# Kernel optimization log

Hardware: AMD Instinct MI355X
Metric: run time of the kernel (lower is better)

## Reference

```python
import jax, jax.numpy as jnp
import numpy as np

EPS = 1e-6

def _layernorm(x):
    mu = jnp.mean(x, axis=-1, keepdims=True)
    var = jnp.mean(jnp.square(x - mu), axis=-1, keepdims=True)
    return (x - mu) / jnp.sqrt(var + EPS)

def setup_inputs() -> dict:
    key = jax.random.key(0)
    ks = jax.random.split(key, 12)
    B, N, C = 4, 1024, 1024
    H = 16
    Dff = 4 * C
    s = 0.02
    x = jax.random.normal(ks[0], (B, N, C), dtype=jnp.float32)
    mask = jax.random.randint(ks[1], (N, N), 0, 2) > 0  # True = attend
    wq = jax.random.normal(ks[2], (C, C), dtype=jnp.float32) * s
    bq = jnp.zeros((C,), dtype=jnp.float32)
    wkv = jax.random.normal(ks[3], (C, 2 * C), dtype=jnp.float32) * s
    bkv = jnp.zeros((2 * C,), dtype=jnp.float32)
    wo = jax.random.normal(ks[4], (C, C), dtype=jnp.float32) * s
    bo = jnp.zeros((C,), dtype=jnp.float32)
    w1 = jax.random.normal(ks[5], (C, Dff), dtype=jnp.float32) * s
    b1 = jnp.zeros((Dff,), dtype=jnp.float32)
    w2 = jax.random.normal(ks[6], (Dff, C), dtype=jnp.float32) * s
    b2 = jnp.zeros((C,), dtype=jnp.float32)
    return {"x": x, "mask": mask, "wq": wq, "bq": bq, "wkv": wkv, "bkv": bkv,
            "wo": wo, "bo": bo, "w1": w1, "b1": b1, "w2": w2, "b2": b2}

def reference(x, mask, wq, bq, wkv, bkv, wo, bo, w1, b1, w2, b2):
    B, N, C = x.shape
    H = 16
    d = C // H
    scale = d ** -0.5
    max_neg = -jnp.finfo(x.dtype).max
    # attn_bias: 0 where mask True, -max where False; broadcast [1,1,N,N]
    attn_bias = jnp.where(mask, jnp.asarray(0.0, x.dtype), jnp.asarray(max_neg, x.dtype))[None, None]

    # --- pre-norm attention ---
    xn = _layernorm(x)
    q = (xn @ wq + bq).reshape(B, N, H, d)
    kv = xn @ wkv + bkv
    k, v = jnp.split(kv, 2, axis=-1)
    k = k.reshape(B, N, H, d)
    v = v.reshape(B, N, H, d)
    sim = jnp.einsum('bihd,bjhd->bhij', q, k) * scale + attn_bias
    attn = jax.nn.softmax(sim, axis=-1)
    o = jnp.einsum('bhij,bjhd->bihd', attn, v).reshape(B, N, C)
    x = x + (o @ wo + bo)

    # --- pre-norm MLP with tanh-approx GELU ---
    xn = _layernorm(x)
    h = jax.nn.gelu(xn @ w1 + b1, approximate=True)
    x = x + (h @ w2 + b2)
    return x
```

## Files before the change

kernel.cpp:

```cpp
#include <hip/hip_runtime.h>
#include <hip/hip_bf16.h>

typedef short bf16x8 __attribute__((ext_vector_type(8)));
typedef float f32x4 __attribute__((ext_vector_type(4)));
typedef unsigned short u16x8 __attribute__((ext_vector_type(8)));

#define MFMA16(a,b,c) __builtin_amdgcn_mfma_f32_16x16x32_bf16((a),(b),(c),0,0,0)

__device__ inline unsigned short f32_to_bf16(float f){
  union { float f; unsigned u; } v; v.f = f;
  unsigned u = v.u;
  u += 0x7FFFu + ((u >> 16) & 1u);
  return (unsigned short)(u >> 16);
}
__device__ inline float bf16_to_f32(unsigned short u){
  union { unsigned u; float f; } v; v.u = ((unsigned)u)<<16; return v.f;
}

__device__ inline float gelu_tanh(float x){
  float x3 = x*x*x;
  float t = tanhf(0.7978845608028654f*(x + 0.044715f*x3));
  return 0.5f*x*(1.0f+t);
}

__device__ inline void gload16(const void* g, void* l){
  __builtin_amdgcn_global_load_lds(
      (const __attribute__((address_space(1))) void*)g,
      (__attribute__((address_space(3))) void*)l, 16, 0, 0);
}

__device__ inline int xcd_swz(int lin, int nwg){
  int cpx = nwg >> 3;
  return (lin & 7)*cpx + (lin >> 3);
}

__global__ void detect_mask_kernel(const unsigned* __restrict__ m, int* __restrict__ flag){
  __shared__ int s;
  if (threadIdx.x == 0) s = 0;
  __syncthreads();
  unsigned w = m[threadIdx.x];
  if (w > 1u) atomicOr(&s, 1);
  __syncthreads();
  if (threadIdx.x == 0) *flag = s;
}

__global__ __launch_bounds__(256) void mask_bias_kernel(
    const void* __restrict__ mask, const int* __restrict__ flag,
    unsigned short* __restrict__ biasr){
  __shared__ float mt[16][64];
  int qg = blockIdx.x, jt = blockIdx.y;
  int t = threadIdx.x;
  int fl = *flag;
  int jc = jt*64 + (t&63);
  #pragma unroll
  for (int k2=0;k2<4;k2++){
    int qr = qg*16 + (t>>6) + k2*4;
    bool a = fl ? (((const unsigned char*)mask)[(size_t)qr*1024 + jc] != 0)
                : (((const int*)mask)[(size_t)qr*1024 + jc] != 0);
    mt[(t>>6)+k2*4][t&63] = a ? -23.083120654223414f : -1e30f;
  }
  __syncthreads();
  ushort4 ob;
  unsigned short tmp[4];
  #pragma unroll
  for (int u=0;u<4;u++){
    int p = t*4+u;
    int e = p&15, lane = p>>4;
    int i = e>>2, jj = e&3;
    int ln2 = lane&15, g2 = lane>>4;
    tmp[u] = f32_to_bf16(mt[g2*4+i][jj*16+ln2]);
  }
  ob.x=tmp[0]; ob.y=tmp[1]; ob.z=tmp[2]; ob.w=tmp[3];
  *(ushort4*)&biasr[((size_t)(qg*16+jt)*64)*16 + t*4] = ob;
}

__global__ __launch_bounds__(256) void transpose_cvt_kernel(
    const float* __restrict__ W, unsigned short* __restrict__ WT, int K, int N){
  __shared__ float tile[32][37];
  int n0 = blockIdx.x*32, k0 = blockIdx.y*32;
  int r = threadIdx.x>>3, c4 = threadIdx.x&7;
  float4 v = *(const float4*)&W[(size_t)(k0+r)*N + n0 + c4*4];
  tile[r][c4*4+0]=v.x; tile[r][c4*4+1]=v.y; tile[r][c4*4+2]=v.z; tile[r][c4*4+3]=v.w;
  __syncthreads();
  ushort4 o;
  o.x = f32_to_bf16(tile[c4*4+0][r]);
  o.y = f32_to_bf16(tile[c4*4+1][r]);
  o.z = f32_to_bf16(tile[c4*4+2][r]);
  o.w = f32_to_bf16(tile[c4*4+3][r]);
  *(ushort4*)&WT[(size_t)(n0+r)*K + k0 + c4*4] = o;
}

__global__ __launch_bounds__(256) void vtrans_kernel(
    const unsigned short* __restrict__ qkv, unsigned short* __restrict__ vt){
  __shared__ unsigned short t[32][33];
  int b = blockIdx.z;
  int n0 = blockIdx.x*32, d0 = blockIdx.y*32;
  int tx = threadIdx.x & 31, ty = threadIdx.x >> 5;
  #pragma unroll
  for (int r=0;r<4;r++)
    t[ty+8*r][tx] = qkv[(size_t)(b*1024 + n0+ty+8*r)*3072 + 2048 + d0+tx];
  __syncthreads();
  #pragma unroll
  for (int r=0;r<4;r++)
    vt[((size_t)b<<20) + (size_t)(d0+ty+8*r)*1024 + n0+tx] = t[tx][ty+8*r];
}

__global__ void bias_concat_kernel(const float* __restrict__ bq,
                                   const float* __restrict__ bkv,
                                   float* __restrict__ dst){
  int i = blockIdx.x*256 + threadIdx.x;
  if (i < 3072) dst[i] = (i < 1024) ? bq[i] : bkv[i-1024];
}

__global__ __launch_bounds__(256) void ln_kernel(const float* __restrict__ x,
                                                 unsigned short* __restrict__ xn){
  const int C = 1024;
  size_t row = blockIdx.x;
  float4 v = reinterpret_cast<const float4*>(x + row*C)[threadIdx.x];
  float s = v.x+v.y+v.z+v.w;
  float q = v.x*v.x+v.y*v.y+v.z*v.z+v.w*v.w;
  #pragma unroll
  for (int off=32; off; off>>=1){ s += __shfl_xor(s,off); q += __shfl_xor(q,off); }
  __shared__ float sm[8];
  int wv = threadIdx.x>>6, ln = threadIdx.x&63;
  if (ln==0){ sm[wv]=s; sm[4+wv]=q; }
  __syncthreads();
  float S = sm[0]+sm[1]+sm[2]+sm[3];
  float Q = sm[4]+sm[5]+sm[6]+sm[7];
  float mu  = S*(1.0f/1024.0f);
  float var = Q*(1.0f/1024.0f) - mu*mu;
  float inv = rsqrtf(var + 1e-6f);
  ushort4 o;
  o.x = f32_to_bf16((v.x-mu)*inv);
  o.y = f32_to_bf16((v.y-mu)*inv);
  o.z = f32_to_bf16((v.z-mu)*inv);
  o.w = f32_to_bf16((v.w-mu)*inv);
  reinterpret_cast<ushort4*>(xn + row*C)[threadIdx.x] = o;
}

template<int EPI>
__global__ __launch_bounds__(256) void gemm64_kernel(
    const unsigned short* __restrict__ A,
    const unsigned short* __restrict__ BT,
    const float* __restrict__ bias,
    const float* __restrict__ resid,
    void* __restrict__ Cout,
    int M, int N, int K)
{
  __shared__ __align__(16) unsigned short lA[2][128*32];
  __shared__ __align__(16) unsigned short lB[2][64*32];
  int tid = threadIdx.x, wave = tid>>6, lane = tid&63;
  int nbx = gridDim.x;
  int lin = blockIdx.y*nbx + blockIdx.x;
  int w = xcd_swz(lin, nbx*gridDim.y);
  int m0 = (w/nbx)*128, n0 = (w%nbx)*64;
  int ln = lane&15, g = lane>>4;

  int srow = wave*16 + (lane>>2);
  int scol = (lane&3)*8;
  const unsigned short* gA0 = A  + (size_t)(m0+srow)*K    + scol;
  const unsigned short* gA1 = A  + (size_t)(m0+64+srow)*K + scol;
  const unsigned short* gB0 = BT + (size_t)(n0+srow)*K    + scol;
  int lof0 = wave*512;
  int lof1 = 64*32 + wave*512;

  f32x4 acc[4][2] = {};
  int wm = wave>>1, wn = wave&1;

  int nt = K/32;
  gload16(gA0, &lA[0][lof0]);
  gload16(gA1, &lA[0][lof1]);
  gload16(gB0, &lB[0][lof0]);
  __syncthreads();
  int cur = 0;
  for (int t=0; t<nt; ++t){
    if (t+1 < nt){
      int ko = (t+1)*32;
      gload16(gA0+ko, &lA[cur^1][lof0]);
      gload16(gA1+ko, &lA[cur^1][lof1]);
      gload16(gB0+ko, &lB[cur^1][lof0]);
    }
    bf16x8 a[4], b[2];
    const unsigned short* pA = &lA[cur][(wm*64+ln)*32 + g*8];
    const unsigned short* pB = &lB[cur][(wn*32+ln)*32 + g*8];
    #pragma unroll
    for (int i=0;i<4;i++) a[i] = *(const bf16x8*)(pA + i*16*32);
    #pragma unroll
    for (int i=0;i<2;i++) b[i] = *(const bf16x8*)(pB + i*16*32);
    #pragma unroll
    for (int mi=0;mi<4;mi++)
      #pragma unroll
      for (int ni=0;ni<2;ni++)
        acc[mi][ni] = MFMA16(a[mi], b[ni], acc[mi][ni]);
    __syncthreads();
    cur ^= 1;
  }

  #pragma unroll
  for (int mi=0;mi<4;mi++){
    int r0 = m0 + wm*64 + mi*16 + g*4;
    #pragma unroll
    for (int ni=0;ni<2;ni++){
      int c = n0 + wn*32 + ni*16 + ln;
      float bs = bias[c];
      f32x4 cc = acc[mi][ni];
      #pragma unroll
      for (int i=0;i<4;i++){
        int r = r0 + i;
        float v = cc[i] + bs;
        if (EPI == 1){
          v += resid[(size_t)r*N + c];
          ((float*)Cout)[(size_t)r*N + c] = v;
        } else if (EPI == 2){
          ((unsigned short*)Cout)[(size_t)r*N + c] = f32_to_bf16(gelu_tanh(v));
        } else {
          ((unsigned short*)Cout)[(size_t)r*N + c] = f32_to_bf16(v);
        }
      }
    }
  }
}

template<int EPI>
__global__ __launch_bounds__(512) void gemm8_kernel(
    const unsigned short* __restrict__ A,
    const unsigned short* __restrict__ BT,
    const float* __restrict__ bias,
    void* __restrict__ Cout,
    int M, int N, int K)
{
  extern __shared__ __align__(16) char smem[];
  const int tid = threadIdx.x, wave = tid>>6, lane = tid&63;
  const int ln = lane&15, g = lane>>4;
  const int wm = wave>>2, wn = wave&3;
  const int nbx = gridDim.x;
  const int lin = blockIdx.y*nbx + blockIdx.x;
  const int wsw = xcd_swz(lin, nbx*gridDim.y);
  const int m0 = (wsw/nbx)*256, n0 = (wsw%nbx)*256;
  const int NT = K>>6;
  const int axor = (g*16) ^ (((ln>>2)&3)<<4);

  auto STAGE = [&](int kt, int h){
    const bool isB = h&1; const int kh = h>>1;
    const unsigned short* src = isB ? BT : A;
    const int base0 = isB ? n0 : m0;
    char* region = smem + (isB?65536:0) + (kt&1)*32768 + kh*16384;
    #pragma unroll
    for (int r=0;r<2;r++){
      int idx = r*512 + tid;
      int row = idx>>2;
      int col = kt*64 + kh*32 + ((((idx&3)*16) ^ (((row>>2)&3)<<4))>>1);
      gload16(src + (size_t)(base0+row)*K + col,
              region + (r*512 + wave*64)*16);
    }
  };

  STAGE(0,0); STAGE(0,1); STAGE(0,2); STAGE(0,3);
  STAGE(1,0); STAGE(1,1); STAGE(1,2);
  asm volatile("s_waitcnt vmcnt(6)" ::: "memory");
  __builtin_amdgcn_s_barrier();
  __builtin_amdgcn_sched_barrier(0);

  f32x4 acc[8][4] = {};
  bf16x8 a[8], b[2];

  for (int t=0; t<NT; ++t){
    const int cur = t&1;
    char* Ac0 = smem + cur*32768;
    char* Ac1 = Ac0 + 16384;
    char* Bc0 = smem + 65536 + cur*32768;
    char* Bc1 = Bc0 + 16384;
    #pragma unroll
    for (int mi=0;mi<8;mi++)
      a[mi] = *(const bf16x8*)(Ac0 + (wm*128+mi*16+ln)*64 + axor);
    b[0] = *(const bf16x8*)(Bc0 + (wn*64+ 0+ln)*64 + axor);
    b[1] = *(const bf16x8*)(Bc0 + (wn*64+16+ln)*64 + axor);
    if (t+1 < NT) STAGE(t+1,3);
    __builtin_amdgcn_s_barrier();
    __builtin_amdgcn_s_setprio(1);
    #pragma unroll
    for (int mi=0;mi<8;mi++){
      acc[mi][0] = MFMA16(a[mi], b[0], acc[mi][0]);
      acc[mi][1] = MFMA16(a[mi], b[1], acc[mi][1]);
    }
    __builtin_amdgcn_s_setprio(0);
    __builtin_amdgcn_s_barrier();
    b[0] = *(const bf16x8*)(Bc0 + (wn*64+32+ln)*64 + axor);
    b[1] = *(const bf16x8*)(Bc0 + (wn*64+48+ln)*64 + axor);
    if (t+2 < NT) STAGE(t+2,0);
    __builtin_amdgcn_s_barrier();
    __builtin_amdgcn_s_setprio(1);
    #pragma unroll
    for (int mi=0;mi<8;mi++){
      acc[mi][2] = MFMA16(a[mi], b[0], acc[mi][2]);
      acc[mi][3] = MFMA16(a[mi], b[1], acc[mi][3]);
    }
    __builtin_amdgcn_s_setprio(0);
    __builtin_amdgcn_s_barrier();
    #pragma unroll
    for (int mi=0;mi<8;mi++)
      a[mi] = *(const bf16x8*)(Ac1 + (wm*128+mi*16+ln)*64 + axor);
    b[0] = *(const bf16x8*)(Bc1 + (wn*64+ 0+ln)*64 + axor);
    b[1] = *(const bf16x8*)(Bc1 + (wn*64+16+ln)*64 + axor);
    if (t+2 < NT) STAGE(t+2,1);
    __builtin_amdgcn_s_barrier();
    __builtin_amdgcn_s_setprio(1);
    #pragma unroll
    for (int mi=0;mi<8;mi++){
      acc[mi][0] = MFMA16(a[mi], b[0], acc[mi][0]);
      acc[mi][1] = MFMA16(a[mi], b[1], acc[mi][1]);
    }
    __builtin_amdgcn_s_setprio(0);
    __builtin_amdgcn_s_barrier();
    b[0] = *(const bf16x8*)(Bc1 + (wn*64+32+ln)*64 + axor);
    b[1] = *(const bf16x8*)(Bc1 + (wn*64+48+ln)*64 + axor);
    if (t+2 < NT) STAGE(t+2,2);
    __builtin_amdgcn_s_barrier();
    __builtin_amdgcn_s_setprio(1);
    #pragma unroll
    for (int mi=0;mi<8;mi++){
      acc[mi][2] = MFMA16(a[mi], b[0], acc[mi][2]);
      acc[mi][3] = MFMA16(a[mi], b[1], acc[mi][3]);
    }
    __builtin_amdgcn_s_setprio(0);
    if (t+2 < NT) asm volatile("s_waitcnt vmcnt(6)" ::: "memory");
    else          asm volatile("s_waitcnt vmcnt(0)" ::: "memory");
    __builtin_amdgcn_s_barrier();
    __builtin_amdgcn_sched_barrier(0);
  }

  #pragma unroll
  for (int mi=0;mi<8;mi++){
    int r0 = m0 + wm*128 + mi*16 + g*4;
    #pragma unroll
    for (int nj=0;nj<4;nj++){
      int c = n0 + wn*64 + nj*16 + ln;
      float bs = bias[c];
      f32x4 cc = acc[mi][nj];
      #pragma unroll
      for (int i=0;i<4;i++){
        int r = r0 + i;
        float v = cc[i] + bs;
        if (EPI == 2){
          ((unsigned short*)Cout)[(size_t)r*N + c] = f32_to_bf16(gelu_tanh(v));
        } else {
          ((unsigned short*)Cout)[(size_t)r*N + c] = f32_to_bf16(v);
        }
      }
    }
  }
}

__global__ __launch_bounds__(256,6) void attn_kernel(
    const unsigned short* __restrict__ qkv,
    const unsigned short* __restrict__ vt,
    const unsigned short* __restrict__ biasr,
    unsigned short* __restrict__ pn,
    float* __restrict__ lsumg)
{
  const int N = 1024, NK = 3072;
  const float SCL = 0.18033688011112042f;
  __shared__ __align__(16) unsigned short lK[64*64];
  __shared__ __align__(16) unsigned short lV[64*64];
  __shared__ __align__(16) unsigned short plds[4][16][72];
  int bh = blockIdx.x, qt = blockIdx.y, sp = blockIdx.z;
  int b = bh>>4, h = bh&15;
  int tid = threadIdx.x, wave = tid>>6, lane = tid&63;
  int ln = lane&15, g = lane>>4;
  size_t base = (size_t)b*N;
  int q_local = qt*64 + wave*16;

  const unsigned short* qptr = qkv + (base + q_local + ln)*NK + h*64;
  bf16x8 aq0 = *(const bf16x8*)(qptr + g*8);
  bf16x8 aq1 = *(const bf16x8*)(qptr + 32 + g*8);

  int r0s = tid>>3,        c0 = (tid&7) ^ (r0s&7);
  int r1s = 32 + (tid>>3), c1 = (tid&7) ^ (r1s&7);
  const unsigned short* kg0 = qkv + (base + r0s)*NK + 1024 + h*64 + c0*8;
  const unsigned short* kg1 = qkv + (base + r1s)*NK + 1024 + h*64 + c1*8;
  const unsigned short* vg0 = vt + ((size_t)b<<20) + (size_t)(h*64 + r0s)*N + c0*8;
  const unsigned short* vg1 = vt + ((size_t)b<<20) + (size_t)(h*64 + r1s)*N + c1*8;
  char* lKd0 = (char*)lK + (wave*64)*16;
  char* lKd1 = (char*)lK + (256 + wave*64)*16;
  char* lVd0 = (char*)lV + (wave*64)*16;
  char* lVd1 = (char*)lV + (256 + wave*64)*16;

  const unsigned short* brp = biasr +
      (((size_t)(qt*4 + wave)*16)*64 + lane)*16;

  f32x4 oacc[4] = {};
  float lsum[4] = {0.f,0.f,0.f,0.f};
  const int xl = (ln&7);

  for (int t=0; t<8; ++t){
    int j0 = sp*512 + t*64;
    __syncthreads();
    gload16(kg0 + (size_t)j0*NK, lKd0);
    gload16(kg1 + (size_t)j0*NK, lKd1);
    gload16(vg0 + j0, lVd0);
    gload16(vg1 + j0, lVd1);
    int jt = j0>>6;
    bf16x8 bb0 = *(const bf16x8*)(brp + (size_t)jt*1024);
    bf16x8 bb1 = *(const bf16x8*)(brp + (size_t)jt*1024 + 8);
    asm volatile("s_waitcnt vmcnt(0)" ::: "memory");
    __builtin_amdgcn_s_barrier();

    f32x4 s[4];
    #pragma unroll
    for (int jj=0;jj<4;jj++){
      int row = jj*16+ln;
      bf16x8 k0 = *(const bf16x8*)((const char*)lK + row*128 + ((g^xl)<<4));
      bf16x8 k1 = *(const bf16x8*)((const char*)lK + row*128 + (((g+4)^xl)<<4));
      s[jj] = (f32x4){};
      s[jj] = MFMA16(aq0, k0, s[jj]);
      s[jj] = MFMA16(aq1, k1, s[jj]);
    }
    #pragma unroll
    for (int i=0;i<4;i++){
      #pragma unroll
      for (int jj=0;jj<4;jj++){
        int e = i*4+jj;
        unsigned short bu = (e<8) ? (unsigned short)bb0[e] : (unsigned short)bb1[e-8];
        float ev = exp2f(fmaf(s[jj][i], SCL, bf16_to_f32(bu)));
        lsum[i] += ev;
        plds[wave][4*g+i][jj*16+ln] = f32_to_bf16(ev);
      }
    }
    asm volatile("s_waitcnt lgkmcnt(0)" ::: "memory");
    __builtin_amdgcn_sched_barrier(0);
    bf16x8 p0 = *(const bf16x8*)&plds[wave][ln][g*8];
    bf16x8 p1 = *(const bf16x8*)&plds[wave][ln][32 + g*8];
    #pragma unroll
    for (int nd=0;nd<4;nd++){
      int row = nd*16+ln;
      bf16x8 v0 = *(const bf16x8*)((const char*)lV + row*128 + ((g^xl)<<4));
      bf16x8 v1 = *(const bf16x8*)((const char*)lV + row*128 + (((g+4)^xl)<<4));
      oacc[nd] = MFMA16(p0, v0, oacc[nd]);
      oacc[nd] = MFMA16(p1, v1, oacc[nd]);
    }
  }

  #pragma unroll
  for (int i=0;i<4;i++){
    float l = lsum[i];
    l += __shfl_xor(l,1); l += __shfl_xor(l,2);
    l += __shfl_xor(l,4); l += __shfl_xor(l,8);
    if (ln == 0)
      lsumg[((size_t)sp<<16) + (size_t)(base + q_local + 4*g + i)*16 + h] = l;
  }
  #pragma unroll
  for (int nd=0;nd<4;nd++){
    #pragma unroll
    for (int i=0;i<4;i++){
      int qr = q_local + 4*g + i;
      pn[((size_t)sp<<22) + (base+qr)*1024 + h*64 + nd*16 + ln] = f32_to_bf16(oacc[nd][i]);
    }
  }
}

__global__ __launch_bounds__(256) void attn_reduce_kernel(
    const unsigned short* __restrict__ pn,
    const float* __restrict__ lsumg,
    unsigned short* __restrict__ o)
{
  size_t idx = ((size_t)blockIdx.x*256 + threadIdx.x)*8;
  int r = (int)(idx>>10);
  int h = (int)((idx&1023)>>6);
  float inv = 1.0f/(lsumg[(size_t)r*16+h] + lsumg[(1u<<16) + (size_t)r*16+h]);
  u16x8 p0 = *(const u16x8*)(pn + idx);
  u16x8 p1 = *(const u16x8*)(pn + (1u<<22) + idx);
  u16x8 res;
  #pragma unroll
  for (int e=0;e<8;e++)
    res[e] = f32_to_bf16((bf16_to_f32((unsigned short)p0[e]) +
                          bf16_to_f32((unsigned short)p1[e]))*inv);
  *(u16x8*)(o + idx) = res;
}

extern "C" void kernel_launch(void* const* d_in, const int* in_sizes, int n_in,
                              void* d_out, int out_size, void* d_ws, size_t ws_size,
                              hipStream_t stream)
{
  (void)in_sizes; (void)n_in; (void)out_size; (void)ws_size;
  const float* x   = (const float*)d_in[0];
  const void*  mask= d_in[1];
  const float* wq  = (const float*)d_in[2];
  const float* bq  = (const float*)d_in[3];
  const float* wkv = (const float*)d_in[4];
  const float* bkv = (const float*)d_in[5];
  const float* wo  = (const float*)d_in[6];
  const float* bo  = (const float*)d_in[7];
  const float* w1  = (const float*)d_in[8];
  const float* b1  = (const float*)d_in[9];
  const float* w2  = (const float*)d_in[10];
  const float* b2  = (const float*)d_in[11];
  float* out = (float*)d_out;

  char* ws = (char*)d_ws;
  size_t off = 0;
  auto alloc = [&](size_t bytes){ size_t o = off; off += (bytes + 255) & ~(size_t)255; return o; };
  unsigned short* WqkvT = (unsigned short*)(ws + alloc(3072u*1024u*2));
  unsigned short* WoT   = (unsigned short*)(ws + alloc(1024u*1024u*2));
  unsigned short* W1T   = (unsigned short*)(ws + alloc(4096u*1024u*2));
  unsigned short* W2T   = (unsigned short*)(ws + alloc(1024u*4096u*2));
  float*          BIASQ = (float*)(ws + alloc(3072u*4));
  int*            FLAG  = (int*)(ws + alloc(256));
  float*          LSUM  = (float*)(ws + alloc(2u*4096u*16u*4));
  unsigned short* BIASR = (unsigned short*)(ws + alloc(64u*16u*64u*16u*2));
  unsigned short* XN    = (unsigned short*)(ws + alloc(4096u*1024u*2));
  float*          X1    = (float*)(ws + alloc(4096u*1024u*4));
  unsigned short* QKV   = (unsigned short*)(ws + alloc(4096u*4096u*2));
  unsigned short* VT    = QKV + (size_t)4096u*3072u;
  unsigned short* PN    = (unsigned short*)X1;

  hipFuncSetAttribute(reinterpret_cast<const void*>(&gemm8_kernel<0>),
                      hipFuncAttributeMaxDynamicSharedMemorySize, 131072);
  hipFuncSetAttribute(reinterpret_cast<const void*>(&gemm8_kernel<2>),
                      hipFuncAttributeMaxDynamicSharedMemorySize, 131072);

  transpose_cvt_kernel<<<dim3(32,32),  256, 0, stream>>>(wq,  WqkvT,               1024, 1024);
  transpose_cvt_kernel<<<dim3(64,32),  256, 0, stream>>>(wkv, WqkvT + 1024u*1024u, 1024, 2048);
  transpose_cvt_kernel<<<dim3(32,32),  256, 0, stream>>>(wo,  WoT,                 1024, 1024);
  transpose_cvt_kernel<<<dim3(128,32), 256, 0, stream>>>(w1,  W1T,                 1024, 4096);
  transpose_cvt_kernel<<<dim3(32,128), 256, 0, stream>>>(w2,  W2T,                 4096, 1024);
  bias_concat_kernel<<<12, 256, 0, stream>>>(bq, bkv, BIASQ);
  detect_mask_kernel<<<1, 256, 0, stream>>>((const unsigned*)mask, FLAG);
  mask_bias_kernel<<<dim3(64,16), 256, 0, stream>>>(mask, FLAG, BIASR);

  ln_kernel<<<4096, 256, 0, stream>>>(x, XN);
  gemm8_kernel<0><<<dim3(12,16), 512, 131072, stream>>>(XN, WqkvT, BIASQ, QKV, 4096, 3072, 1024);
  vtrans_kernel<<<dim3(32,32,4), 256, 0, stream>>>(QKV, VT);
  attn_kernel<<<dim3(64,16,2), 256, 0, stream>>>(QKV, VT, BIASR, PN, LSUM);
  attn_reduce_kernel<<<2048, 256, 0, stream>>>(PN, LSUM, XN);
  gemm64_kernel<1><<<dim3(16,32), 256, 0, stream>>>(XN, WoT, bo, x, X1, 4096, 1024, 1024);
  ln_kernel<<<4096, 256, 0, stream>>>(X1, XN);
  gemm8_kernel<2><<<dim3(16,16), 512, 131072, stream>>>(XN, W1T, b1, QKV, 4096, 4096, 1024);
  gemm64_kernel<1><<<dim3(16,32), 256, 0, stream>>>(QKV, W2T, b2, X1, out, 4096, 1024, 4096);
}
```

Measured before the change: 273.3 us.

## Triple-buffer GEMM LDS tiles with explicit vmcnt waits for deeper prefetch

Turns the double-buffered K-loop of the 128x64 bf16 GEMM into a three-stage pipeline. Up to three tiles are in flight, and explicit s_waitcnt vmcnt counts replace the full __syncthreads, so the loop waits only for the oldest stage. The aim is to hide global-load latency better. In exchange it uses 50% more shared memory per block, which can cut occupancy. Correctness now depends on the hand-counted vmcnt values matching the direct-to-LDS load instructions per stage, and STAGE(1) and STAGE(2) are issued unconditionally, so K/32 must be at least 3.

Result: no change. 269.4 us (-1.4%).

```diff
diff --git a/kernel.cpp b/kernel.cpp
--- a/kernel.cpp
+++ b/kernel.cpp
@@ -147,8 +147,8 @@
     void* __restrict__ Cout,
     int M, int N, int K)
 {
-  __shared__ __align__(16) unsigned short lA[2][128*32];
-  __shared__ __align__(16) unsigned short lB[2][64*32];
+  __shared__ __align__(16) unsigned short lA[3][128*32];
+  __shared__ __align__(16) unsigned short lB[3][64*32];
   int tid = threadIdx.x, wave = tid>>6, lane = tid&63;
   int nbx = gridDim.x;
   int lin = blockIdx.y*nbx + blockIdx.x;
@@ -166,23 +166,28 @@
 
   f32x4 acc[4][2] = {};
   int wm = wave>>1, wn = wave&1;
-
   int nt = K/32;
-  gload16(gA0, &lA[0][lof0]);
-  gload16(gA1, &lA[0][lof1]);
-  gload16(gB0, &lB[0][lof0]);
-  __syncthreads();
-  int cur = 0;
+
+  auto STAGE = [&](int t, int buf){
+    int ko = t*32;
+    gload16(gA0+ko, &lA[buf][lof0]);
+    gload16(gA1+ko, &lA[buf][lof1]);
+    gload16(gB0+ko, &lB[buf][lof0]);
+  };
+
+  STAGE(0,0); STAGE(1,1); STAGE(2,2);
+
+  int cb = 0;
   for (int t=0; t<nt; ++t){
-    if (t+1 < nt){
-      int ko = (t+1)*32;
-      gload16(gA0+ko, &lA[cur^1][lof0]);
-      gload16(gA1+ko, &lA[cur^1][lof1]);
-      gload16(gB0+ko, &lB[cur^1][lof0]);
-    }
+    int rem = nt-1-t;
+    if (rem >= 2)      asm volatile("s_waitcnt vmcnt(6)" ::: "memory");
+    else if (rem == 1) asm volatile("s_waitcnt vmcnt(3)" ::: "memory");
+    else               asm volatile("s_waitcnt vmcnt(0)" ::: "memory");
+    __builtin_amdgcn_s_barrier();
+
     bf16x8 a[4], b[2];
-    const unsigned short* pA = &lA[cur][(wm*64+ln)*32 + g*8];
-    const unsigned short* pB = &lB[cur][(wn*32+ln)*32 + g*8];
+    const unsigned short* pA = &lA[cb][(wm*64+ln)*32 + g*8];
+    const unsigned short* pB = &lB[cb][(wn*32+ln)*32 + g*8];
     #pragma unroll
     for (int i=0;i<4;i++) a[i] = *(const bf16x8*)(pA + i*16*32);
     #pragma unroll
@@ -192,8 +197,11 @@
       #pragma unroll
       for (int ni=0;ni<2;ni++)
         acc[mi][ni] = MFMA16(a[mi], b[ni], acc[mi][ni]);
-    __syncthreads();
-    cur ^= 1;
+
+    asm volatile("s_waitcnt lgkmcnt(0)" ::: "memory");
+    __builtin_amdgcn_s_barrier();
+    if (t+3 < nt) STAGE(t+3, cb);
+    cb = (cb==2) ? 0 : cb+1;
   }
 
   #pragma unroll
```
